# Kernel tuning notes

Hardware: AMD Instinct MI355X
Metric: run time of the kernel (lower is better)

The kernel has to match this reference:

```python
import jax, jax.numpy as jnp
import numpy as np

# dims: L blocks, S cur_seq, M memory_len, B batch, D embed, H heads, IN input_dim
L, S, M, B, D, H, IN = 4, 512, 512, 8, 1024, 16, 128
HD = D // H
GRU_BIAS = 2.0  # config['gru_bias']


def _ln(x, s, b, eps=1e-5):
    mu = x.mean(-1, keepdims=True)
    var = ((x - mu) ** 2).mean(-1, keepdims=True)
    return (x - mu) * jax.lax.rsqrt(var + eps) * s + b


def _pos_emb(full_seq, dim):
    # SinusoidalPE: freqs = arange(0, dim, 2.0); inv = 10000**(-freqs/dim); seq descending
    freqs = jnp.arange(0, dim, 2.0)
    inv = 10000.0 ** (-freqs / dim)
    seq = jnp.arange(full_seq - 1, -1, -1.0)
    ang = seq[:, None] * inv[None, :]
    return jnp.concatenate([jnp.sin(ang), jnp.cos(ang)], axis=-1)  # (F, dim)


def _rel_shift(x):
    # x: (q, k, b, h) -> Transformer-XL relative shift
    q, k, b, h = x.shape
    xp = jnp.pad(x, ((0, 0), (1, 0), (0, 0), (0, 0)))
    return xp.reshape(k + 1, q, b, h)[1:].reshape(q, k, b, h)


def _gru(x, y, Wr, Ur, Wz, Uz, Wg, Ug):
    r = jax.nn.sigmoid(y @ Wr + x @ Ur)
    z = jax.nn.sigmoid(y @ Wz + x @ Uz - GRU_BIAS)
    hcand = jnp.tanh(y @ Wg + (r * x) @ Ug)
    return (1.0 - z) * x + z * hcand


def setup_inputs() -> dict:
    key = jax.random.key(0)
    ks = iter(jax.random.split(key, 64))

    def mat(*shape):
        return jax.random.normal(next(ks), shape, jnp.float32) * (shape[-2] ** -0.5)

    return dict(
        h=jax.random.normal(next(ks), (B, S, IN), jnp.float32),
        memory=jnp.zeros((L, M, B, D), jnp.float32),
        We=mat(IN, D), be=jnp.zeros((D,), jnp.float32),
        ln1_s=jnp.ones((L, D), jnp.float32), ln1_b=jnp.zeros((L, D), jnp.float32),
        ln2_s=jnp.ones((L, D), jnp.float32), ln2_b=jnp.zeros((L, D), jnp.float32),
        Wq=mat(L, D, D), bq=jnp.zeros((L, D), jnp.float32),
        Wk=mat(L, D, D), bk=jnp.zeros((L, D), jnp.float32),
        Wv=mat(L, D, D), bv=jnp.zeros((L, D), jnp.float32),
        Wr=mat(L, D, D), br=jnp.zeros((L, D), jnp.float32),
        Wo=mat(L, D, D), bo=jnp.zeros((L, D), jnp.float32),
        u=jax.random.normal(next(ks), (L, H, HD), jnp.float32) * 0.02,
        vb=jax.random.normal(next(ks), (L, H, HD), jnp.float32) * 0.02,
        gWr=mat(L, 2, D, D), gUr=mat(L, 2, D, D),
        gWz=mat(L, 2, D, D), gUz=mat(L, 2, D, D),
        gWg=mat(L, 2, D, D), gUg=mat(L, 2, D, D),
        fW1=mat(L, D, 4 * D), fb1=jnp.zeros((L, 4 * D), jnp.float32),
        fW2=mat(L, 4 * D, D), fb2=jnp.zeros((L, D), jnp.float32),
    )


def reference(h, memory, We, be, ln1_s, ln1_b, ln2_s, ln2_b,
              Wq, bq, Wk, bk, Wv, bv, Wr, br, Wo, bo, u, vb,
              gWr, gUr, gWz, gUz, gWg, gUg, fW1, fb1, fW2, fb2):
    x = jnp.transpose(h, (1, 0, 2))                      # (S, B, IN)
    x = jax.nn.gelu(x @ We + be, approximate=False)      # (S, B, D)
    F = S + M
    pos = _pos_emb(F, D)                                 # (F, D)
    mask = jnp.triu(jnp.ones((S, F), bool), k=1 + M)     # (S, F)
    scale = HD ** -0.5
    out = x
    for i in range(L):
        full = jnp.concatenate([memory[i], out], axis=0)  # (F, B, D)
        qn = _ln(out, ln1_s[i], ln1_b[i])
        kn = _ln(full, ln1_s[i], ln1_b[i])
        q = (qn @ Wq[i] + bq[i]).reshape(S, B, H, HD)
        k = (kn @ Wk[i] + bk[i]).reshape(F, B, H, HD)
        v = (kn @ Wv[i] + bv[i]).reshape(F, B, H, HD)
        r = (pos @ Wr[i] + br[i]).reshape(F, H, HD)
        content = jnp.einsum('ibhd,jbhd->ijbh', q + u[i], k)
        position = _rel_shift(jnp.einsum('ibhd,jhd->ijbh', q + vb[i], r))
        attn = (content + position) * scale               # (S, F, B, H)
        attn = jnp.where(mask[:, :, None, None], -1e30, attn)
        a = jax.nn.softmax(attn, axis=1)
        y = jnp.einsum('ijbh,jbhd->ibhd', a, v).reshape(S, B, D) @ Wo[i] + bo[i]
        y = jax.nn.gelu(y, approximate=False)
        out1 = _gru(out, y, gWr[i, 0], gUr[i, 0], gWz[i, 0], gUz[i, 0], gWg[i, 0], gUg[i, 0])
        e = _ln(out1, ln2_s[i], ln2_b[i])
        e = jax.nn.gelu(e @ fW1[i] + fb1[i], approximate=False)
        e = jax.nn.gelu(e @ fW2[i] + fb2[i], approximate=False)
        out = _gru(out1, e, gWr[i, 1], gUr[i, 1], gWz[i, 1], gUz[i, 1], gWg[i, 1], gUg[i, 1])
    return jnp.transpose(out, (1, 0, 2))                  # (B, S, D)
```

## Files before the change

### kernel.cpp

```cpp
#include <hip/hip_runtime.h>

typedef unsigned short u16;
typedef unsigned long long u64;
typedef __attribute__((ext_vector_type(8))) short bf16x8;
typedef __attribute__((ext_vector_type(4))) float f32x4;

#define DEVI __device__ __forceinline__

#define KSC 0.1803368801111244f

DEVI u16 f2b(float f) {
  unsigned u = __float_as_uint(f);
  u += 0x7fffu + ((u >> 16) & 1u);
  return (u16)(u >> 16);
}
DEVI float b2f(u16 v) { return __uint_as_float((unsigned)v << 16); }
DEVI unsigned cvtpk(float lo, float hi) {
  unsigned r;
  asm("v_cvt_pk_bf16_f32 %0, %1, %2" : "=v"(r) : "v"(lo), "v"(hi));
  return r;
}
DEVI float tanh_f(float x) {
  float xc = fminf(fmaxf(x, -15.f), 15.f);
  float e = __expf(2.f * xc);
  return (e - 1.f) / (e + 1.f);
}
DEVI float gelu_f(float x) {
  float u = 0.7978845608028654f * x * (1.f + 0.044715f * x * x);
  return 0.5f * x * (1.f + tanh_f(u));
}
DEVI float sigm_f(float x) { return 1.f / (1.f + __expf(-x)); }

DEVI void gload16(const void* g, void* l) {
  __builtin_amdgcn_global_load_lds((__attribute__((address_space(1))) void*)g,
                                   (__attribute__((address_space(3))) void*)l, 16, 0, 0);
}

template <int NT, int BN>
__global__ __launch_bounds__(NT) void gemm_bt(
    const u16* __restrict__ A, const u16* __restrict__ Bt,
    const float* __restrict__ bias, const float* __restrict__ bias2,
    float* __restrict__ C32, u16* __restrict__ C16, u16* __restrict__ C16b,
    int M, int N, int K, int ldA, int ldB, int ldC,
    long long sA, long long sBb, long long sBh, long long sC, int nH, int flags)
{
  constexpr int WN = BN / 32;
  constexpr int RA = (128 * 8) / NT;
  constexpr int RB = (BN * 8) / NT;
  __shared__ __align__(16) u16 Sm[2][(128 + BN) * 64];
  const int z = blockIdx.z;
  const int zb = z / nH, zh = z - zb * nH;
  A  += (long long)z * sA;
  Bt += (long long)zb * sBb + (long long)zh * sBh;
  const long long cOff = (long long)z * sC;
  const int m0 = blockIdx.x * 128, n0 = blockIdx.y * BN;
  const int t = threadIdx.x, lane = t & 63;
  const int w = t >> 6;
  const int wm = (w / WN) * 64, wn = (w % WN) * 32;

  f32x4 acc[4][2];
#pragma unroll
  for (int i = 0; i < 4; ++i)
#pragma unroll
    for (int j = 0; j < 2; ++j) { f32x4 zz = {0.f, 0.f, 0.f, 0.f}; acc[i][j] = zz; }

  auto stage = [&](int buf, int k0) {
#pragma unroll
    for (int r = 0; r < RA; ++r) {
      const int c = r * NT + t;
      const int row = c >> 3;
      const int col = (c & 7) << 3;
      int ga = m0 + row; if (ga >= M) ga = M - 1;
      gload16(A + (long long)ga * ldA + (k0 + col),
              &Sm[buf][(size_t)(r * NT + (t & (NT - 64))) * 8]);
    }
#pragma unroll
    for (int r = 0; r < RB; ++r) {
      const int c = r * NT + t;
      const int row = c >> 3;
      const int col = (c & 7) << 3;
      int gb = n0 + row; if (gb >= N) gb = N - 1;
      gload16(Bt + (long long)gb * ldB + (k0 + col),
              &Sm[buf][(size_t)(1024 + r * NT + (t & (NT - 64))) * 8]);
    }
  };

  auto compute = [&](int buf) {
    const u16* As = &Sm[buf][0];
    const u16* Bs = &Sm[buf][128 * 64];
#pragma unroll
    for (int ks = 0; ks < 2; ++ks) {
      const int ko = ks * 32 + ((lane >> 4) << 3);
      bf16x8 af[4], bfv[2];
#pragma unroll
      for (int i = 0; i < 4; ++i)
        af[i] = *(const bf16x8*)&As[(wm + i * 16 + (lane & 15)) * 64 + ko];
#pragma unroll
      for (int i = 0; i < 2; ++i)
        bfv[i] = *(const bf16x8*)&Bs[(wn + i * 16 + (lane & 15)) * 64 + ko];
#pragma unroll
      for (int mi = 0; mi < 4; ++mi)
#pragma unroll
        for (int ni = 0; ni < 2; ++ni)
          acc[mi][ni] = __builtin_amdgcn_mfma_f32_16x16x32_bf16(af[mi], bfv[ni], acc[mi][ni], 0, 0, 0);
    }
  };

  stage(0, 0);
  __syncthreads();
  int cur = 0;
  for (int k0 = 64; k0 < K; k0 += 64) {
    stage(cur ^ 1, k0);
    compute(cur);
    __syncthreads();
    cur ^= 1;
  }
  compute(cur);

  const int cb = n0 + wn + (lane & 15);
  const int rb = m0 + wm + ((lane >> 4) << 2);
#pragma unroll
  for (int ni = 0; ni < 2; ++ni) {
    const int col = cb + ni * 16;
    if (col >= N) continue;
    float bv = 0.f;
    if (flags & 2) bv = ((flags & 128) && zh) ? bias2[col] : bias[col];
#pragma unroll
    for (int mi = 0; mi < 4; ++mi) {
#pragma unroll
      for (int q = 0; q < 4; ++q) {
        const int row = rb + mi * 16 + q;
        if (row >= M) continue;
        float x = acc[mi][ni][q] + bv;
        if (flags & 1) x = gelu_f(x);
        if (flags & 64) {
          const long long o = ((long long)((row & 7) * 16 + (col >> 6)) * ldC + (row >> 3)) * 64 + (col & 63);
          C16[o] = f2b(x * KSC);
          C16b[o] = f2b((x + bias2[col]) * KSC);
        } else if (flags & 128) {
          if (zh == 0) {
            const long long o = ((long long)((row & 7) * 16 + (col >> 6)) * ldC + (row >> 3)) * 64 + (col & 63);
            C16[o] = f2b(x);
          } else {
            C16b[(long long)row * 1024 + col] = f2b(x);
          }
        } else {
          long long o;
          if (flags & 16)
            o = ((long long)((row & 7) * 16 + (col >> 6)) * ldC + (row >> 3)) * 64 + (col & 63);
          else if (flags & 32)
            o = ((long long)(col >> 6) * 1024 + row) * 64 + (col & 63);
          else
            o = cOff + (long long)row * ldC + col;
          if (flags & 4) C32[o] = x;
          if (flags & 8) C16[o] = f2b(x);
        }
      }
    }
  }
}

__global__ __launch_bounds__(256) void fused_attn(
    const u16* __restrict__ Qu,
    const u16* __restrict__ Qv,
    const u16* __restrict__ Kb,
    const u16* __restrict__ Vt,
    const u16* __restrict__ Rh,
    u16* __restrict__ Y)
{
  constexpr int F = 1024;
  const int bid = blockIdx.x;
  const int wk = (bid & 7) * 128 + (bid >> 3);
  const int i0 = (wk & 7) * 64;
  const int bh = wk >> 3;
  const int h = bh & 15;

  __shared__ __align__(16) u16 Ks[2][64 * 64];
  __shared__ __align__(16) u16 Vs[2][64 * 64];
  __shared__ __align__(16) u16 Rs[2][64 * 64];
  __shared__ __align__(8) u16 PBT[2][64 * 68];
  __shared__ __align__(16) u16 Ps[4][16][72];

  const int t = threadIdx.x;
  const int lane = t & 63;
  const int wq = t >> 6;
  const int l15 = lane & 15, lhi = lane >> 4;

  const u16* QUg = Qu + ((size_t)bh * 512 + i0) * 64;
  const u16* QVg = Qv + ((size_t)bh * 512 + i0) * 64;
  const u16* Kg = Kb + (size_t)bh * F * 64;
  const u16* Vg = Vt + (size_t)bh * 64 * F;
  const u16* Rg = Rh + (size_t)h * F * 64;

  bf16x8 au[2], av[2];
#pragma unroll
  for (int ks = 0; ks < 2; ++ks) {
    const int arow = wq * 16 + l15;
    au[ks] = *(const bf16x8*)(QUg + arow * 64 + ks * 32 + lhi * 8);
    av[ks] = *(const bf16x8*)(QVg + arow * 64 + ks * 32 + lhi * 8);
  }

  auto stageT = [&](const u16* g, u16* dst) {
#pragma unroll
    for (int rnd = 0; rnd < 2; ++rnd) {
      const int idx = rnd * 256 + t;
      const int row = idx >> 3;
      const int gs = (idx & 7) ^ (row & 7);
      gload16(g + row * 64 + gs * 8, dst + (size_t)(rnd * 256 + (t & 192)) * 8);
    }
  };
  auto stageVf = [&](int j0, u16* dst) {
#pragma unroll
    for (int rnd = 0; rnd < 2; ++rnd) {
      const int idx = rnd * 256 + t;
      const int row = idx >> 3;
      const int gs = (idx & 7) ^ (row & 7);
      gload16(Vg + (size_t)row * F + j0 + gs * 8, dst + (size_t)(rnd * 256 + (t & 192)) * 8);
    }
  };

  const int nT = i0 / 64 + 9;

  stageT(Kg, Ks[0]);
  stageVf(0, Vs[0]);
  stageT(Rg + (size_t)(512 - i0) * 64, Rs[0]);
  stageT(Rg + (size_t)(448 - i0) * 64, Rs[1]);
  __syncthreads();
  {
    f32x4 pb0[4];
#pragma unroll
    for (int i = 0; i < 4; ++i) { f32x4 zz = {0.f, 0.f, 0.f, 0.f}; pb0[i] = zz; }
    __builtin_amdgcn_s_setprio(1);
#pragma unroll
    for (int ks = 0; ks < 2; ++ks)
#pragma unroll
      for (int ni = 0; ni < 4; ++ni) {
        const int brow = ni * 16 + l15;
        const bf16x8 br_ = *(const bf16x8*)&Rs[1][brow * 64 + (((ks * 4 + lhi) ^ (brow & 7)) << 3)];
        pb0[ni] = __builtin_amdgcn_mfma_f32_16x16x32_bf16(av[ks], br_, pb0[ni], 0, 0, 0);
      }
    __builtin_amdgcn_s_setprio(0);
#pragma unroll
    for (int ni = 0; ni < 4; ++ni) {
      u64 w = (u64)cvtpk(pb0[ni][0], pb0[ni][1]) | ((u64)cvtpk(pb0[ni][2], pb0[ni][3]) << 32);
      *(u64*)&PBT[0][(size_t)(ni * 16 + l15) * 68 + wq * 16 + lhi * 4] = w;
    }
  }
  __syncthreads();

  f32x4 Oacc[4];
#pragma unroll
  for (int i = 0; i < 4; ++i) { f32x4 zz = {0.f, 0.f, 0.f, 0.f}; Oacc[i] = zz; }
  float mrow[4] = {-3.0e38f, -3.0e38f, -3.0e38f, -3.0e38f};
  float lrow[4] = {0.f, 0.f, 0.f, 0.f};

  for (int st = 0; st < nT; ++st) {
    const int b = st & 1;
    const bool lastT = (st == nT - 1);

    if (!lastT) {
      const int j1 = (st + 1) * 64;
      stageT(Kg + (size_t)j1 * 64, Ks[b ^ 1]);
      stageVf(j1, Vs[b ^ 1]);
      if (st + 1 < nT - 1)
        stageT(Rg + (size_t)(j1 - i0 + 512) * 64, Rs[b ^ 1]);
    }

    f32x4 cacc[4], pbh[4];
#pragma unroll
    for (int i = 0; i < 4; ++i) {
      f32x4 zz = {0.f, 0.f, 0.f, 0.f};
      cacc[i] = zz; pbh[i] = zz;
    }
    __builtin_amdgcn_s_setprio(1);
#pragma unroll
    for (int ks = 0; ks < 2; ++ks) {
#pragma unroll
      for (int ni = 0; ni < 4; ++ni) {
        const int brow = ni * 16 + l15;
        const bf16x8 bk_ = *(const bf16x8*)&Ks[b][brow * 64 + (((ks * 4 + lhi) ^ (brow & 7)) << 3)];
        cacc[ni] = __builtin_amdgcn_mfma_f32_16x16x32_bf16(au[ks], bk_, cacc[ni], 0, 0, 0);
      }
      if (!lastT) {
#pragma unroll
        for (int ni = 0; ni < 4; ++ni) {
          const int brow = ni * 16 + l15;
          const bf16x8 br_ = *(const bf16x8*)&Rs[b][brow * 64 + (((ks * 4 + lhi) ^ (brow & 7)) << 3)];
          pbh[ni] = __builtin_amdgcn_mfma_f32_16x16x32_bf16(av[ks], br_, pbh[ni], 0, 0, 0);
        }
      }
    }
    __builtin_amdgcn_s_setprio(0);

    if (!lastT) {
#pragma unroll
      for (int ni = 0; ni < 4; ++ni) {
        u64 w = (u64)cvtpk(pbh[ni][0], pbh[ni][1]) | ((u64)cvtpk(pbh[ni][2], pbh[ni][3]) << 32);
        *(u64*)&PBT[(st + 1) & 1][(size_t)(ni * 16 + l15) * 68 + wq * 16 + lhi * 4] = w;
      }
    }

    const u16* pbLo = &PBT[st & 1][0];
    const u16* pbHi = &PBT[(st + 1) & 1][0];
    float sc[4][4];
#pragma unroll
    for (int ni = 0; ni < 4; ++ni) {
      const int dj = ni * 16 + l15;
#pragma unroll
      for (int qq = 0; qq < 4; ++qq) {
        const int di = wq * 16 + lhi * 4 + qq;
        const int cc = dj - di + 63;
        const float pb = b2f((cc < 64) ? pbLo[(size_t)cc * 68 + di]
                                       : pbHi[(size_t)(cc - 64) * 68 + di]);
        float s = cacc[ni][qq] + pb;
        if (lastT && dj > di) s = -1e30f;
        sc[ni][qq] = s;
      }
    }

    float r4[4];
    float dmax = -3.0e38f;
#pragma unroll
    for (int qq = 0; qq < 4; ++qq) {
      float r = fmaxf(fmaxf(sc[0][qq], sc[1][qq]), fmaxf(sc[2][qq], sc[3][qq]));
      r = fmaxf(r, __shfl_xor(r, 1));
      r = fmaxf(r, __shfl_xor(r, 2));
      r = fmaxf(r, __shfl_xor(r, 4));
      r = fmaxf(r, __shfl_xor(r, 8));
      r4[qq] = r;
      dmax = fmaxf(dmax, r - mrow[qq]);
    }
    const bool skip = __all(dmax <= 8.f);
    if (!skip) {
#pragma unroll
      for (int qq = 0; qq < 4; ++qq) {
        const float nm = fmaxf(mrow[qq], r4[qq]);
        const float esc = exp2f(mrow[qq] - nm);
        mrow[qq] = nm;
        lrow[qq] *= esc;
#pragma unroll
        for (int nd = 0; nd < 4; ++nd) Oacc[nd][qq] *= esc;
      }
    }
    float ps[4][4];
    float rsum[4] = {0.f, 0.f, 0.f, 0.f};
#pragma unroll
    for (int ni = 0; ni < 4; ++ni)
#pragma unroll
      for (int qq = 0; qq < 4; ++qq) {
        float p = exp2f(sc[ni][qq] - mrow[qq]);
        ps[ni][qq] = p;
        rsum[qq] += p;
      }
#pragma unroll
    for (int qq = 0; qq < 4; ++qq) {
      float r = rsum[qq];
      r += __shfl_xor(r, 1);
      r += __shfl_xor(r, 2);
      r += __shfl_xor(r, 4);
      r += __shfl_xor(r, 8);
      lrow[qq] += r;
    }

#pragma unroll
    for (int ni = 0; ni < 4; ++ni) {
      unsigned p01 = cvtpk(ps[ni][0], ps[ni][1]);
      unsigned p23 = cvtpk(ps[ni][2], ps[ni][3]);
      Ps[wq][lhi * 4 + 0][ni * 16 + l15] = (u16)p01;
      Ps[wq][lhi * 4 + 1][ni * 16 + l15] = (u16)(p01 >> 16);
      Ps[wq][lhi * 4 + 2][ni * 16 + l15] = (u16)p23;
      Ps[wq][lhi * 4 + 3][ni * 16 + l15] = (u16)(p23 >> 16);
    }
    __builtin_amdgcn_s_setprio(1);
#pragma unroll
    for (int ks = 0; ks < 2; ++ks) {
      const bf16x8 pa = *(const bf16x8*)&Ps[wq][l15][ks * 32 + lhi * 8];
#pragma unroll
      for (int nd = 0; nd < 4; ++nd) {
        const int vrow = nd * 16 + l15;
        const bf16x8 vb_ = *(const bf16x8*)&Vs[b][vrow * 64 + (((ks * 4 + lhi) ^ (vrow & 7)) << 3)];
        Oacc[nd] = __builtin_amdgcn_mfma_f32_16x16x32_bf16(pa, vb_, Oacc[nd], 0, 0, 0);
      }
    }
    __builtin_amdgcn_s_setprio(0);

    __syncthreads();
  }

  float inv[4];
#pragma unroll
  for (int qq = 0; qq < 4; ++qq) inv[qq] = 1.f / lrow[qq];
  const int b = bh >> 4;
  const int rbase = i0 + wq * 16 + lhi * 4;
#pragma unroll
  for (int nd = 0; nd < 4; ++nd) {
    const int d = nd * 16 + l15;
    unsigned w01 = cvtpk(Oacc[nd][0] * inv[0], Oacc[nd][1] * inv[1]);
    unsigned w23 = cvtpk(Oacc[nd][2] * inv[2], Oacc[nd][3] * inv[3]);
    u16* yb = Y + (size_t)rbase * 8192 + b * 1024 + h * 64 + d;
    yb[0] = (u16)w01; yb[8192] = (u16)(w01 >> 16);
    yb[16384] = (u16)w23; yb[24576] = (u16)(w23 >> 16);
  }
}

__global__ __launch_bounds__(256) void biasprep(const float* __restrict__ bq,
                                                const float* __restrict__ u,
                                                const float* __restrict__ vb,
                                                float* __restrict__ bqu,
                                                float* __restrict__ dvb)
{
  const int i = blockIdx.x * 256 + threadIdx.x;
  bqu[i] = bq[i] + u[i];
  dvb[i] = vb[i] - u[i];
}

#define MAXW 20
struct WPack {
  const float* src[MAXW];
  u16* dst[MAXW];
  int K[MAXW], N[MAXW];
  int tilePrefix[MAXW + 1];
  int nm;
};

__global__ __launch_bounds__(256) void wtrans_kernel(WPack p) {
  int bid = blockIdx.x;
  int m = 0;
  while (m < p.nm && bid >= p.tilePrefix[m + 1]) ++m;
  if (m >= p.nm) return;
  const int lt = bid - p.tilePrefix[m];
  const int K = p.K[m], N = p.N[m];
  const int tN = N >> 5;
  const int kt = lt / tN, nt = lt - kt * tN;
  const int k0 = kt << 5, n0 = nt << 5;
  const float* src = p.src[m];
  u16* dst = p.dst[m];
  __shared__ float tile[32][33];
  const int t = threadIdx.x;
  const int r = t >> 3, c4 = (t & 7) << 2;
  float4 v = *(const float4*)&src[(size_t)(k0 + r) * N + n0 + c4];
  tile[r][c4 + 0] = v.x; tile[r][c4 + 1] = v.y; tile[r][c4 + 2] = v.z; tile[r][c4 + 3] = v.w;
  __syncthreads();
  u16 o0 = f2b(tile[c4 + 0][r]);
  u16 o1 = f2b(tile[c4 + 1][r]);
  u16 o2 = f2b(tile[c4 + 2][r]);
  u16 o3 = f2b(tile[c4 + 3][r]);
  u64 w = (u64)o0 | ((u64)o1 << 16) | ((u64)o2 << 32) | ((u64)o3 << 48);
  *(u64*)&dst[(size_t)(n0 + r) * K + k0 + c4] = w;
}

__global__ __launch_bounds__(256) void ln_kernel(
    const float* __restrict__ Xmem, const float* __restrict__ Xout, int rowsMem,
    const float* __restrict__ sc, const float* __restrict__ bi, u16* __restrict__ dst)
{
  const int row = blockIdx.x;
  const float* src = (row < rowsMem) ? (Xmem + (long long)row * 1024)
                                     : (Xout + (long long)(row - rowsMem) * 1024);
  const int t = threadIdx.x;
  float4 v = *(const float4*)&src[t * 4];
  float s1 = v.x + v.y + v.z + v.w;
  float s2 = v.x * v.x + v.y * v.y + v.z * v.z + v.w * v.w;
#pragma unroll
  for (int o = 32; o > 0; o >>= 1) { s1 += __shfl_down(s1, o); s2 += __shfl_down(s2, o); }
  __shared__ float red[8];
  const int wv = t >> 6;
  if ((t & 63) == 0) { red[wv * 2] = s1; red[wv * 2 + 1] = s2; }
  __syncthreads();
  s1 = red[0] + red[2] + red[4] + red[6];
  s2 = red[1] + red[3] + red[5] + red[7];
  const float mu = s1 * (1.f / 1024.f);
  const float var = s2 * (1.f / 1024.f) - mu * mu;
  const float rs = rsqrtf(var + 1e-5f);
  float vals[4] = {v.x, v.y, v.z, v.w};
  u16 o4[4];
#pragma unroll
  for (int j = 0; j < 4; ++j) {
    const int c = t * 4 + j;
    o4[j] = f2b((vals[j] - mu) * rs * sc[c] + bi[c]);
  }
  *(u64*)&dst[(long long)row * 1024 + t * 4] =
      (u64)o4[0] | ((u64)o4[1] << 16) | ((u64)o4[2] << 32) | ((u64)o4[3] << 48);
}

__global__ __launch_bounds__(256) void prep_vt16(const u16* __restrict__ Vf, u16* __restrict__ VT)
{
  const int f0 = blockIdx.x * 64;
  const int bh = blockIdx.y;
  const int b = bh >> 4, h = bh & 15;
  __shared__ u16 tl[64 * 65];
  const int t = threadIdx.x;
  {
    const int fr = t >> 2, c0 = (t & 3) * 16;
    const u16* src = Vf + ((size_t)(f0 + fr) * 8 + b) * 1024 + h * 64 + c0;
    bf16x8 v0 = *(const bf16x8*)src;
    bf16x8 v1 = *(const bf16x8*)(src + 8);
#pragma unroll
    for (int j = 0; j < 8; ++j) tl[fr * 65 + c0 + j] = (u16)v0[j];
#pragma unroll
    for (int j = 0; j < 8; ++j) tl[fr * 65 + c0 + 8 + j] = (u16)v1[j];
  }
  __syncthreads();
  {
    const int dr = t >> 2, c0 = (t & 3) * 16;
    u16* dst = VT + ((long long)bh * 64 + dr) * 1024 + f0 + c0;
#pragma unroll
    for (int j = 0; j < 16; ++j) dst[j] = tl[(c0 + j) * 65 + dr];
  }
}

__global__ __launch_bounds__(256) void pe_kernel(u16* __restrict__ PEB)
{
  const long long idx = (long long)blockIdx.x * 256 + threadIdx.x;
  const int p = (int)(idx >> 10);
  const int d = idx & 1023;
  const int q = d & 511;
  const float inv = powf(10000.f, -(float)(2 * q) * (1.f / 1024.f));
  const float ang = (float)(1023 - p) * inv;
  PEB[idx] = f2b((d < 512) ? sinf(ang) : cosf(ang));
}

__global__ __launch_bounds__(256) void embed_conv(const float* __restrict__ h, u16* __restrict__ A)
{
  const long long idx = (long long)blockIdx.x * 256 + threadIdx.x;
  const int c = idx & 127;
  const int r = (int)(idx >> 7);
  const int s = r >> 3, b = r & 7;
  A[idx] = f2b(h[(((long long)b * 512 + s) << 7) + c]);
}

__global__ __launch_bounds__(256) void gru_elemA(const u16* __restrict__ T1, u16* __restrict__ T2,
                                                 const float* __restrict__ X, u16* __restrict__ RXBF)
{
  const long long i8 = ((long long)blockIdx.x * 256 + threadIdx.x) * 8;
  const int row = (int)(i8 >> 10);
  const int c = i8 & 1023;
  const u16* t1 = T1 + (long long)row * 3072 + c;
  u16* t2 = T2 + (long long)row * 2048 + c;
  bf16x8 ry = *(const bf16x8*)t1;
  bf16x8 zy = *(const bf16x8*)(t1 + 1024);
  bf16x8 rx = *(const bf16x8*)t2;
  bf16x8 zx = *(const bf16x8*)(t2 + 1024);
  float4 x0 = *(const float4*)(X + i8);
  float4 x1 = *(const float4*)(X + i8 + 4);
  float xs[8] = {x0.x, x0.y, x0.z, x0.w, x1.x, x1.y, x1.z, x1.w};
  u16 ro[8], zo[8];
#pragma unroll
  for (int j = 0; j < 8; ++j) {
    float r = sigm_f(b2f((u16)ry[j]) + b2f((u16)rx[j]));
    float z = sigm_f(b2f((u16)zy[j]) + b2f((u16)zx[j]) - 2.f);
    ro[j] = f2b(r * xs[j]);
    zo[j] = f2b(z);
  }
  *(u64*)&RXBF[i8] = (u64)ro[0] | ((u64)ro[1] << 16) | ((u64)ro[2] << 32) | ((u64)ro[3] << 48);
  *(u64*)&RXBF[i8 + 4] = (u64)ro[4] | ((u64)ro[5] << 16) | ((u64)ro[6] << 32) | ((u64)ro[7] << 48);
  *(u64*)&t2[0] = (u64)zo[0] | ((u64)zo[1] << 16) | ((u64)zo[2] << 32) | ((u64)zo[3] << 48);
  *(u64*)&t2[4] = (u64)zo[4] | ((u64)zo[5] << 16) | ((u64)zo[6] << 32) | ((u64)zo[7] << 48);
}

__global__ __launch_bounds__(256) void gru_elemB(const u16* __restrict__ T1, const u16* __restrict__ T2,
                                                 const u16* __restrict__ TG, const float* __restrict__ X,
                                                 float* __restrict__ O, u16* __restrict__ XBF, int tOut)
{
  const long long i8 = ((long long)blockIdx.x * 256 + threadIdx.x) * 8;
  const int row = (int)(i8 >> 10);
  const int c = i8 & 1023;
  bf16x8 gy = *(const bf16x8*)(T1 + (long long)row * 3072 + 2048 + c);
  bf16x8 tt = *(const bf16x8*)(TG + i8);
  bf16x8 zz = *(const bf16x8*)(T2 + (long long)row * 2048 + c);
  float4 x0 = *(const float4*)(X + i8);
  float4 x1 = *(const float4*)(X + i8 + 4);
  float xs[8] = {x0.x, x0.y, x0.z, x0.w, x1.x, x1.y, x1.z, x1.w};
  float os[8];
  u16 ob[8];
#pragma unroll
  for (int j = 0; j < 8; ++j) {
    float z = b2f((u16)zz[j]);
    float o = (1.f - z) * xs[j] + z * tanh_f(b2f((u16)gy[j]) + b2f((u16)tt[j]));
    os[j] = o;
    ob[j] = f2b(o);
  }
  float4 o0 = {os[0], os[1], os[2], os[3]};
  float4 o1 = {os[4], os[5], os[6], os[7]};
  long long oo = i8;
  if (tOut) {
    const int s = row >> 3, b = row & 7;
    oo = (((long long)b * 512 + s) << 10) + c;
  }
  *(float4*)(O + oo) = o0;
  *(float4*)(O + oo + 4) = o1;
  *(u64*)&XBF[i8] = (u64)ob[0] | ((u64)ob[1] << 16) | ((u64)ob[2] << 32) | ((u64)ob[3] << 48);
  *(u64*)&XBF[i8 + 4] = (u64)ob[4] | ((u64)ob[5] << 16) | ((u64)ob[6] << 32) | ((u64)ob[7] << 48);
}

extern "C" void kernel_launch(void* const* d_in, const int* in_sizes, int n_in,
                              void* d_out, int out_size, void* d_ws, size_t ws_size,
                              hipStream_t stream)
{
  (void)in_sizes; (void)n_in; (void)out_size; (void)ws_size;
  const float* h_in   = (const float*)d_in[0];
  const float* memory = (const float*)d_in[1];
  const float* We     = (const float*)d_in[2];
  const float* be     = (const float*)d_in[3];
  const float* ln1s   = (const float*)d_in[4];
  const float* ln1b   = (const float*)d_in[5];
  const float* ln2s   = (const float*)d_in[6];
  const float* ln2b   = (const float*)d_in[7];
  const float* Wq     = (const float*)d_in[8];
  const float* bq     = (const float*)d_in[9];
  const float* Wk     = (const float*)d_in[10];
  const float* bk     = (const float*)d_in[11];
  const float* Wv     = (const float*)d_in[12];
  const float* bv     = (const float*)d_in[13];
  const float* Wr     = (const float*)d_in[14];
  const float* br     = (const float*)d_in[15];
  const float* Wo     = (const float*)d_in[16];
  const float* bo     = (const float*)d_in[17];
  const float* uu     = (const float*)d_in[18];
  const float* vbp    = (const float*)d_in[19];
  const float* gWr    = (const float*)d_in[20];
  const float* gUr    = (const float*)d_in[21];
  const float* gWz    = (const float*)d_in[22];
  const float* gUz    = (const float*)d_in[23];
  const float* gWg    = (const float*)d_in[24];
  const float* gUg    = (const float*)d_in[25];
  const float* fW1    = (const float*)d_in[26];
  const float* fb1    = (const float*)d_in[27];
  const float* fW2    = (const float*)d_in[28];
  const float* fb2    = (const float*)d_in[29];

  constexpr int S = 512, MM = 512, B = 8, D = 1024, H = 16, IN = 128, F = 1024;
  constexpr int SB = 4096, FB = 8192;
  constexpr long long DD = (long long)D * D;

  char* ws = (char*)d_ws;
  size_t off = 0;
  auto alloc = [&](size_t bytes) -> size_t {
    size_t o = off; off = (off + bytes + 255) & ~(size_t)255; return o;
  };
  const size_t oWT   = alloc((size_t)25 * DD * 2);
  const size_t oWET  = alloc((size_t)D * IN * 2);
  const size_t oPEB  = alloc((size_t)F * D * 2);
  const size_t oOUT  = alloc((size_t)SB * D * 4);
  const size_t oOUT1 = alloc((size_t)SB * D * 4);
  const size_t oXBF  = alloc((size_t)SB * D * 2);
  const size_t oYBF  = alloc((size_t)SB * D * 2);
  const size_t oYBFA = alloc((size_t)SB * D * 2);
  const size_t oABUF = alloc((size_t)SB * D * 2);
  const size_t oKN   = alloc((size_t)FB * D * 2);
  const size_t oQU   = alloc((size_t)B * H * S * 64 * 2);
  const size_t oQV   = alloc((size_t)B * H * S * 64 * 2);
  const size_t oKBH  = alloc((size_t)B * H * F * 64 * 2);
  const size_t oVT   = alloc((size_t)B * H * F * 64 * 2);
  const size_t oRH   = alloc((size_t)H * F * 64 * 2);
  const size_t oBQU  = alloc((size_t)D * 4);
  const size_t oDVB  = alloc((size_t)D * 4);
  const size_t oUNI  = off;

  u16* WTp   = (u16*)(ws + oWT);
  u16* WETp  = (u16*)(ws + oWET);
  u16* PEBp  = (u16*)(ws + oPEB);
  float* OUTp  = (float*)(ws + oOUT);
  float* OUT1p = (float*)(ws + oOUT1);
  u16* XBFp  = (u16*)(ws + oXBF);
  u16* YBFp  = (u16*)(ws + oYBF);
  u16* YBFAp = (u16*)(ws + oYBFA);
  u16* ABUFp = (u16*)(ws + oABUF);
  u16* KNp   = (u16*)(ws + oKN);
  u16* QUp   = (u16*)(ws + oQU);
  u16* QVp   = (u16*)(ws + oQV);
  u16* KBHp  = (u16*)(ws + oKBH);
  u16* VTp   = (u16*)(ws + oVT);
  u16* RHp   = (u16*)(ws + oRH);
  float* bquP = (float*)(ws + oBQU);
  float* dvbP = (float*)(ws + oDVB);
  u16* VF16p  = (u16*)(ws + oUNI);
  u16* T1p    = (u16*)(ws + oUNI);
  u16* T2p    = (u16*)(ws + oUNI + (size_t)SB * 3 * D * 2 + 256);
  u16* TGp    = (u16*)(ws + oUNI + (size_t)SB * 5 * D * 2 + 512);
  u16* FFNBp  = (u16*)(ws + oUNI);

  auto gemm = [&](const u16* A, const u16* Bt, const float* bias, const float* bias2,
                  float* C32, u16* C16, u16* C16b,
                  int M, int N, int K, int ldA, int ldB, int ldC,
                  long long sA, long long sBb, long long sBh, long long sC, int nH, int Z,
                  int flags) {
    if (M >= 2048 && N >= 2048 && (N % 128) == 0) {
      dim3 grid((M + 127) / 128, N / 128, Z);
      gemm_bt<512, 128><<<grid, 512, 0, stream>>>(A, Bt, bias, bias2, C32, C16, C16b,
                                                  M, N, K, ldA, ldB, ldC,
                                                  sA, sBb, sBh, sC, nH, flags);
    } else {
      dim3 grid((M + 127) / 128, (N + 63) / 64, Z);
      gemm_bt<256, 64><<<grid, 256, 0, stream>>>(A, Bt, bias, bias2, C32, C16, C16b,
                                                 M, N, K, ldA, ldB, ldC,
                                                 sA, sBb, sBh, sC, nH, flags);
    }
  };

  pe_kernel<<<(F * D) / 256, 256, 0, stream>>>(PEBp);
  {
    WPack p{};
    p.nm = 1; p.src[0] = We; p.dst[0] = WETp; p.K[0] = IN; p.N[0] = D;
    p.tilePrefix[0] = 0; p.tilePrefix[1] = (IN / 32) * (D / 32);
    wtrans_kernel<<<p.tilePrefix[1], 256, 0, stream>>>(p);
  }
  embed_conv<<<(SB * IN) / 256, 256, 0, stream>>>(h_in, ABUFp);
  gemm(ABUFp, WETp, be, nullptr, OUTp, XBFp, nullptr, SB, D, IN, IN, IN, D,
       0, 0, 0, 0, 1, 1, 1 | 2 | 4 | 8);

  for (int li = 0; li < 4; ++li) {
    WPack p{};
    int nt = 0, id = 0;
    auto addw = [&](const float* s, u16* d, int K, int N) {
      p.src[id] = s; p.dst[id] = d; p.K[id] = K; p.N[id] = N;
      p.tilePrefix[id] = nt; nt += (K / 32) * (N / 32); ++id;
    };
    addw(Wq + li * DD, WTp + 0 * DD, D, D);
    addw(Wk + li * DD, WTp + 1 * DD, D, D);
    addw(Wv + li * DD, WTp + 2 * DD, D, D);
    addw(Wr + li * DD, WTp + 3 * DD, D, D);
    addw(Wo + li * DD, WTp + 4 * DD, D, D);
    addw(gWr + (li * 2 + 0) * DD, WTp + 5 * DD, D, D);
    addw(gWz + (li * 2 + 0) * DD, WTp + 6 * DD, D, D);
    addw(gWg + (li * 2 + 0) * DD, WTp + 7 * DD, D, D);
    addw(gUr + (li * 2 + 0) * DD, WTp + 8 * DD, D, D);
    addw(gUz + (li * 2 + 0) * DD, WTp + 9 * DD, D, D);
    addw(gUg + (li * 2 + 0) * DD, WTp + 10 * DD, D, D);
    addw(gWr + (li * 2 + 1) * DD, WTp + 11 * DD, D, D);
    addw(gWz + (li * 2 + 1) * DD, WTp + 12 * DD, D, D);
    addw(gWg + (li * 2 + 1) * DD, WTp + 13 * DD, D, D);
    addw(gUr + (li * 2 + 1) * DD, WTp + 14 * DD, D, D);
    addw(gUz + (li * 2 + 1) * DD, WTp + 15 * DD, D, D);
    addw(gUg + (li * 2 + 1) * DD, WTp + 16 * DD, D, D);
    addw(fW1 + li * (long long)D * 4096, WTp + 17 * DD, D, 4096);
    addw(fW2 + li * (long long)4096 * D, WTp + 21 * DD, 4096, D);
    p.tilePrefix[id] = nt; p.nm = id;
    wtrans_kernel<<<nt, 256, 0, stream>>>(p);

    ln_kernel<<<FB, 256, 0, stream>>>(memory + (long long)li * MM * B * D, OUTp, MM * B,
                                      ln1s + li * D, ln1b + li * D, KNp);
    const u16* QN = KNp + (size_t)MM * B * D;

    biasprep<<<4, 256, 0, stream>>>(bq + li * D, uu + li * D, vbp + li * D, bquP, dvbP);
    gemm(QN, WTp + 0 * DD, bquP, dvbP, nullptr, QUp, QVp, SB, D, D, D, D,  S,
         0, 0, 0, 0, 1, 1, 2 | 64);
    gemm(KNp, WTp + 1 * DD, bk + li * D, bv + li * D, nullptr, KBHp, VF16p,
         FB, D, D, D, D,  F, 0, 0, DD, 0, 2, 2, 2 | 128);
    prep_vt16<<<dim3(F / 64, B * H), 256, 0, stream>>>(VF16p, VTp);
    gemm(PEBp, WTp + 3 * DD, br + li * D, nullptr, nullptr, RHp, nullptr,
         F, D, D, D, D, D, 0, 0, 0, 0, 1, 1, 2 | 8 | 32);

    fused_attn<<<dim3((S / 64) * B * H), 256, 0, stream>>>(QUp, QVp, KBHp, VTp, RHp, YBFAp);

    gemm(YBFAp, WTp + 4 * DD, bo + li * D, nullptr, nullptr, YBFp, nullptr,
         SB, D, D, D, D, D, 0, 0, 0, 0, 1, 1, 1 | 2 | 8);

    gemm(YBFp, WTp + 5 * DD, nullptr, nullptr, nullptr, T1p, nullptr,
         SB, 3 * D, D, D, D, 3 * D, 0, 0, 0, 0, 1, 1, 8);
    gemm(XBFp, WTp + 8 * DD, nullptr, nullptr, nullptr, T2p, nullptr,
         SB, 2 * D, D, D, D, 2 * D, 0, 0, 0, 0, 1, 1, 8);
    gru_elemA<<<(SB * D / 8) / 256, 256, 0, stream>>>(T1p, T2p, OUTp, ABUFp);
    gemm(ABUFp, WTp + 10 * DD, nullptr, nullptr, nullptr, TGp, nullptr,
         SB, D, D, D, D, D, 0, 0, 0, 0, 1, 1, 8);
    gru_elemB<<<(SB * D / 8) / 256, 256, 0, stream>>>(T1p, T2p, TGp, OUTp, OUT1p, XBFp, 0);

    ln_kernel<<<SB, 256, 0, stream>>>(OUT1p, OUT1p, SB, ln2s + li * D, ln2b + li * D, ABUFp);
    gemm(ABUFp, WTp + 17 * DD, fb1 + li * 4096, nullptr, nullptr, FFNBp, nullptr,
         SB, 4096, D, D, D, 4096, 0, 0, 0, 0, 1, 1, 1 | 2 | 8);
    gemm(FFNBp, WTp + 21 * DD, fb2 + li * D, nullptr, nullptr, YBFp, nullptr,
         SB, D, 4096, 4096, 4096, D, 0, 0, 0, 0, 1, 1, 1 | 2 | 8);

    gemm(YBFp, WTp + 11 * DD, nullptr, nullptr, nullptr, T1p, nullptr,
         SB, 3 * D, D, D, D, 3 * D, 0, 0, 0, 0, 1, 1, 8);
    gemm(XBFp, WTp + 14 * DD, nullptr, nullptr, nullptr, T2p, nullptr,
         SB, 2 * D, D, D, D, 2 * D, 0, 0, 0, 0, 1, 1, 8);
    gru_elemA<<<(SB * D / 8) / 256, 256, 0, stream>>>(T1p, T2p, OUT1p, ABUFp);
    gemm(ABUFp, WTp + 16 * DD, nullptr, nullptr, nullptr, TGp, nullptr,
         SB, D, D, D, D, D, 0, 0, 0, 0, 1, 1, 8);
    gru_elemB<<<(SB * D / 8) / 256, 256, 0, stream>>>(
        T1p, T2p, TGp, OUT1p, (li == 3) ? (float*)d_out : OUTp, XBFp, (li == 3) ? 1 : 0);
  }
}
```

Baseline: 2.869 ms.

## Triple-buffer the large GEMM tile pipeline with explicit vmcnt waits

```diff
diff --git a/kernel.cpp b/kernel.cpp
--- a/kernel.cpp
+++ b/kernel.cpp
@@ -36,7 +36,7 @@
                                    (__attribute__((address_space(3))) void*)l, 16, 0, 0);
 }
 
-template <int NT, int BN>
+template <int NT, int BN, int NBUF>
 __global__ __launch_bounds__(NT) void gemm_bt(
     const u16* __restrict__ A, const u16* __restrict__ Bt,
     const float* __restrict__ bias, const float* __restrict__ bias2,
@@ -47,7 +47,8 @@
   constexpr int WN = BN / 32;
   constexpr int RA = (128 * 8) / NT;
   constexpr int RB = (BN * 8) / NT;
-  __shared__ __align__(16) u16 Sm[2][(128 + BN) * 64];
+  static_assert(NBUF == 2 || (NBUF == 3 && RA + RB == 4), "vmcnt literal");
+  __shared__ __align__(16) u16 Sm[NBUF][(128 + BN) * 64];
   const int z = blockIdx.z;
   const int zb = z / nH, zh = z - zb * nH;
   A  += (long long)z * sA;
@@ -106,16 +107,39 @@
     }
   };
 
-  stage(0, 0);
-  __syncthreads();
-  int cur = 0;
-  for (int k0 = 64; k0 < K; k0 += 64) {
-    stage(cur ^ 1, k0);
+  if constexpr (NBUF == 2) {
+    stage(0, 0);
+    __syncthreads();
+    int cur = 0;
+    for (int k0 = 64; k0 < K; k0 += 64) {
+      stage(cur ^ 1, k0);
+      compute(cur);
+      __syncthreads();
+      cur ^= 1;
+    }
     compute(cur);
-    __syncthreads();
-    cur ^= 1;
-  }
-  compute(cur);
+  } else {
+    const int nk = K >> 6;
+    stage(0, 0);
+    if (nk > 1) {
+      stage(1, 64);
+      asm volatile("s_waitcnt vmcnt(4)" ::: "memory");
+    } else {
+      asm volatile("s_waitcnt vmcnt(0)" ::: "memory");
+    }
+    __builtin_amdgcn_s_barrier();
+    for (int tt = 0; tt < nk; ++tt) {
+      if (tt + 2 < nk) stage((tt + 2) % 3, (tt + 2) << 6);
+      compute(tt % 3);
+      if (tt + 1 < nk) {
+        if (tt + 2 < nk)
+          asm volatile("s_waitcnt vmcnt(4)" ::: "memory");
+        else
+          asm volatile("s_waitcnt vmcnt(0)" ::: "memory");
+        __builtin_amdgcn_s_barrier();
+      }
+    }
+  }
 
   const int cb = n0 + wn + (lane & 15);
   const int rb = m0 + wm + ((lane >> 4) << 2);
@@ -686,14 +710,14 @@
                   int flags) {
     if (M >= 2048 && N >= 2048 && (N % 128) == 0) {
       dim3 grid((M + 127) / 128, N / 128, Z);
-      gemm_bt<512, 128><<<grid, 512, 0, stream>>>(A, Bt, bias, bias2, C32, C16, C16b,
-                                                  M, N, K, ldA, ldB, ldC,
-                                                  sA, sBb, sBh, sC, nH, flags);
+      gemm_bt<512, 128, 3><<<grid, 512, 0, stream>>>(A, Bt, bias, bias2, C32, C16, C16b,
+                                                     M, N, K, ldA, ldB, ldC,
+                                                     sA, sBb, sBh, sC, nH, flags);
     } else {
       dim3 grid((M + 127) / 128, (N + 63) / 64, Z);
-      gemm_bt<256, 64><<<grid, 256, 0, stream>>>(A, Bt, bias, bias2, C32, C16, C16b,
-                                                 M, N, K, ldA, ldB, ldC,
-                                                 sA, sBb, sBh, sC, nH, flags);
+      gemm_bt<256, 64, 2><<<grid, 256, 0, stream>>>(A, Bt, bias, bias2, C32, C16, C16b,
+                                                    M, N, K, ldA, ldB, ldC,
+                                                    sA, sBb, sBh, sC, nH, flags);
     }
   };
 
```

Result: slower. 3.294 ms (+14.8%).
